# Kernel tuning notes

Hardware: AMD Instinct MI355X
Metric: run time of the kernel (lower is better)

The kernel has to match this reference:

```python
import jax, jax.numpy as jnp
import numpy as np
from jax.scipy.special import logsumexp

# K particles, J proposal candidates, N taxa, R merges done, T current subtrees,
# S sites, A alphabet, D embedding dim
K, J, N, R, T, S, A, D = 128, 4, 64, 32, 32, 256, 4, 64
PRIOR_BL = 0.1       # expected branch length under exponential prior
TEMPERATURE = 1.0


def _gather_nodes(arr, idx):
    # arr: (Z, t, ...); idx: (Z,) -> (Z, ...)  (per-row gather, gather_K)
    i = idx.reshape((-1,) + (1,) * (arr.ndim - 1))
    return jnp.take_along_axis(arr, i, axis=1)[:, 0]


def _replace_with_merged(arr, idx1, idx2, new_val):
    # remove nodes idx1, idx2 from each row (keeping order) and append merged node
    t = arr.shape[1]
    pos = jnp.arange(t)
    removed = (pos[None, :] == idx1[:, None]) | (pos[None, :] == idx2[:, None])
    order = jnp.argsort(removed.astype(jnp.int32), axis=1, stable=True)
    kept = order[:, : t - 2]
    ki = kept.reshape(kept.shape + (1,) * (arr.ndim - 2))
    kept_vals = jnp.take_along_axis(arr, ki, axis=1)
    return jnp.concatenate([kept_vals, new_val[:, None]], axis=1)


def _hash_tree(h1, h2):
    # order-invariant int32 hash combine (wraps on overflow, as intended)
    mn = jnp.minimum(h1, h2)
    mx = jnp.maximum(h1, h2)
    return (mn * 1000003 + mx) * 40503 + 2531011


def _q_matrix(emb_ZxD, W_q):
    # GTR-style rate matrix from merged-node embedding (site-independent decoder)
    logits = (emb_ZxD @ W_q).reshape(-1, A, A)
    off = jax.nn.softplus(logits) * (1.0 - jnp.eye(A, dtype=logits.dtype))
    return off - jnp.eye(A, dtype=logits.dtype) * off.sum(-1, keepdims=True)


def setup_inputs() -> dict:
    key = jax.random.key(0)
    ks = jax.random.split(key, 20)
    merge1_indexes_Kxr = jax.random.randint(ks[0], (K, R), 0, N).astype(jnp.int32)
    merge2_indexes_Kxr = jax.random.randint(ks[1], (K, R), 0, N).astype(jnp.int32)
    branch1_lengths_Kxr = jax.random.uniform(ks[2], (K, R)) * 0.2 + 1e-3
    branch2_lengths_Kxr = jax.random.uniform(ks[3], (K, R)) * 0.2 + 1e-3
    embeddings_KxrxD = jax.random.normal(ks[4], (K, R, D))
    # leaf counts per subtree, summing to N per particle
    lc_row = jnp.concatenate([jnp.full((T // 2,), 1, jnp.int32), jnp.full((T - T // 2,), 3, jnp.int32)])
    leaf_counts_Kxt = jnp.tile(lc_row[None], (K, 1))
    hashes_Kxt = jax.random.randint(ks[5], (K, T), 0, 2 ** 30).astype(jnp.int32)
    embeddings_KxtxD = jax.random.normal(ks[6], (K, T, D))
    log_felsensteins_KxtxSxA = -jax.random.uniform(ks[7], (K, T, S, A)) * 3.0
    log_pi_K = -jax.random.uniform(ks[8], (K,)) * 100.0
    indexes_K = jax.random.randint(ks[9], (K,), 0, K).astype(jnp.int32)
    # proposal outputs (stand-in for the learned proposal): idx1 != idx2
    idx1_KxJ = jax.random.randint(ks[10], (K, J), 0, T).astype(jnp.int32)
    off = jax.random.randint(ks[11], (K, J), 1, T).astype(jnp.int32)
    idx2_KxJ = (idx1_KxJ + off) % T
    branch1_KxJ = jax.random.uniform(ks[12], (K, J)) * 0.2 + 1e-3
    branch2_KxJ = jax.random.uniform(ks[13], (K, J)) * 0.2 + 1e-3
    embedding_KxJxD = jax.random.normal(ks[14], (K, J, D))
    log_v_plus_KxJ = jnp.full((K, J), np.log(T * (T - 1) / 2.0), jnp.float32)
    gumbel_KxJ = jax.random.gumbel(ks[15], (K, J))
    W_q = jax.random.normal(ks[16], (D, A * A)) * 0.05
    W_stat = jax.random.normal(ks[17], (D, A)) * 0.05
    vals = np.zeros(2 * N, dtype=np.float64)
    for i in range(2, 2 * N):
        vals[i] = vals[i - 2] + np.log(i)
    log_double_factorials_2N = jnp.asarray(vals, jnp.float32)
    return {
        'indexes_K': indexes_K,
        'merge1_indexes_Kxr': merge1_indexes_Kxr,
        'merge2_indexes_Kxr': merge2_indexes_Kxr,
        'branch1_lengths_Kxr': branch1_lengths_Kxr,
        'branch2_lengths_Kxr': branch2_lengths_Kxr,
        'embeddings_KxrxD': embeddings_KxrxD,
        'leaf_counts_Kxt': leaf_counts_Kxt,
        'hashes_Kxt': hashes_Kxt,
        'embeddings_KxtxD': embeddings_KxtxD,
        'log_felsensteins_KxtxSxA': log_felsensteins_KxtxSxA,
        'log_pi_K': log_pi_K,
        'idx1_KxJ': idx1_KxJ,
        'idx2_KxJ': idx2_KxJ,
        'branch1_KxJ': branch1_KxJ,
        'branch2_KxJ': branch2_KxJ,
        'embedding_KxJxD': embedding_KxJxD,
        'log_v_plus_KxJ': log_v_plus_KxJ,
        'gumbel_KxJ': gumbel_KxJ,
        'W_q': W_q,
        'W_stat': W_stat,
        'log_double_factorials_2N': log_double_factorials_2N,
    }


def reference(indexes_K, merge1_indexes_Kxr, merge2_indexes_Kxr,
              branch1_lengths_Kxr, branch2_lengths_Kxr, embeddings_KxrxD,
              leaf_counts_Kxt, hashes_Kxt, embeddings_KxtxD,
              log_felsensteins_KxtxSxA, log_pi_K,
              idx1_KxJ, idx2_KxJ, branch1_KxJ, branch2_KxJ,
              embedding_KxJxD, log_v_plus_KxJ, gumbel_KxJ,
              W_q, W_stat, log_double_factorials_2N):
    # ---- ancestor resampling gather (ms[...][indexes_K]) ----
    g = lambda a: a[indexes_K]
    merge1_Kxr = g(merge1_indexes_Kxr); merge2_Kxr = g(merge2_indexes_Kxr)
    b1_Kxr = g(branch1_lengths_Kxr); b2_Kxr = g(branch2_lengths_Kxr)
    emb_KxrxD = g(embeddings_KxrxD)
    lc_Kxt = g(leaf_counts_Kxt); h_Kxt = g(hashes_Kxt)
    emb_KxtxD = g(embeddings_KxtxD)
    lf_KxtxSxA = g(log_felsensteins_KxtxSxA)
    logpi_K = g(log_pi_K)
    # ---- flatten proposal to Z = K*J (hash_trick=False: Z = K*J, no dedup) ----
    Z = K * J
    rep = lambda a: jnp.repeat(a, J, axis=0)  # K_to_Z
    idx1_Z = idx1_KxJ.reshape(Z); idx2_Z = idx2_KxJ.reshape(Z)
    branch1_Z = branch1_KxJ.reshape(Z); branch2_Z = branch2_KxJ.reshape(Z)
    emb_ZxD = embedding_KxJxD.reshape(Z, D)
    log_v_plus_Z = log_v_plus_KxJ.reshape(Z)
    merge1_Z = rep(merge1_Kxr); merge2_Z = rep(merge2_Kxr)
    b1_Z = rep(b1_Kxr); b2_Z = rep(b2_Kxr)
    embr_Z = rep(emb_KxrxD)
    lc_Z = rep(lc_Kxt); h_Z = rep(h_Kxt)
    embt_Z = rep(emb_KxtxD)
    lf_Z = rep(lf_KxtxSxA)
    logpi_Z = rep(logpi_K)
    # ---- append candidate branches ----
    b1_all = jnp.concatenate([b1_Z, branch1_Z[:, None]], axis=1)  # Z x (R+1)
    b2_all = jnp.concatenate([b2_Z, branch2_Z[:, None]], axis=1)
    # ---- merge step ----
    new_lc = _gather_nodes(lc_Z, idx1_Z) + _gather_nodes(lc_Z, idx2_Z)
    new_h = _hash_tree(_gather_nodes(h_Z, idx1_Z), _gather_nodes(h_Z, idx2_Z))
    lc_new = _replace_with_merged(lc_Z, idx1_Z, idx2_Z, new_lc)      # Z x (T-1)
    h_new = _replace_with_merged(h_Z, idx1_Z, idx2_Z, new_h)
    embt_new = _replace_with_merged(embt_Z, idx1_Z, idx2_Z, emb_ZxD)
    # ---- Felsenstein pruning update ----
    Q = _q_matrix(emb_ZxD, W_q)                                      # Z x A x A
    expm = jax.scipy.linalg.expm
    P1 = jax.vmap(expm)(Q * branch1_Z[:, None, None])
    P2 = jax.vmap(expm)(Q * branch2_Z[:, None, None])
    logP1 = jnp.log(jnp.clip(P1, 1e-30))
    logP2 = jnp.log(jnp.clip(P2, 1e-30))
    lf1 = _gather_nodes(lf_Z, idx1_Z)  # Z x S x A
    lf2 = _gather_nodes(lf_Z, idx2_Z)
    new_lf = (logsumexp(logP1[:, None, :, :] + lf1[:, :, None, :], axis=-1)
              + logsumexp(logP2[:, None, :, :] + lf2[:, :, None, :], axis=-1))
    lf_new = _replace_with_merged(lf_Z, idx1_Z, idx2_Z, new_lf)      # Z x (T-1) x S x A
    # ---- stationary probs per node & log pi ----
    log_stat = jax.nn.log_softmax(embt_new @ W_stat, axis=-1)        # Z x (T-1) x A
    ll_nodes = logsumexp(lf_new + log_stat[:, :, None, :], axis=-1).sum(-1)  # Z x (T-1)
    log_lik_Z = ll_nodes.sum(-1)
    rate = 1.0 / PRIOR_BL
    log_branch_prior = ((jnp.log(rate) - rate * b1_all).sum(-1)
                        + (jnp.log(rate) - rate * b2_all).sum(-1))
    df_idx = jnp.clip(2 * lc_new - 3, 0, 2 * N - 1)
    log_topo = -log_double_factorials_2N[df_idx].sum(-1)
    log_pi_new_Z = log_lik_Z + log_branch_prior + log_topo
    log_v_minus_Z = jnp.log(jnp.sum(lc_new > 1, axis=-1).astype(jnp.float32))
    # ---- weights & sub-resampling ----
    log_w_Z = log_pi_new_Z - logpi_Z + log_v_minus_Z - log_v_plus_Z
    log_w_KxJ = log_w_Z.reshape(K, J)
    log_weight_K = logsumexp(log_w_KxJ, axis=1) - jnp.log(float(J))
    sub_idx_K = jnp.argmax(log_w_KxJ / TEMPERATURE + gumbel_KxJ, axis=1)  # Gumbel-max = Categorical sample
    sel = jnp.arange(K) * J + sub_idx_K
    gs = lambda a: a[sel]
    merge1_out = jnp.concatenate([gs(merge1_Z), gs(idx1_Z)[:, None]], axis=1)
    merge2_out = jnp.concatenate([gs(merge2_Z), gs(idx2_Z)[:, None]], axis=1)
    embr_out = jnp.concatenate([gs(embr_Z), gs(emb_ZxD)[:, None, :]], axis=1)
    return (merge1_out, merge2_out, gs(b1_all), gs(b2_all), embr_out,
            gs(lc_new), gs(h_new), gs(embt_new), gs(lf_new),
            gs(log_pi_new_Z), log_weight_K, gs(log_lik_Z))
```

## Files before the change

kernel.cpp:

```cpp
#include <hip/hip_runtime.h>
#include <math.h>

constexpr int K_ = 128, J_ = 4, R_ = 32, T_ = 32, S_ = 256, A_ = 4, D_ = 64;
constexpr int Z_ = K_ * J_;
constexpr int NDF_ = 128;
constexpr float RATE_ = 10.0f;

constexpr int NB_NODE = K_ * T_ / 4;
constexpr int NB_HYP  = Z_ / 4;

constexpr int OFF_M1   = 0;
constexpr int OFF_M2   = OFF_M1 + K_ * 33;
constexpr int OFF_B1   = OFF_M2 + K_ * 33;
constexpr int OFF_B2   = OFF_B1 + K_ * 33;
constexpr int OFF_EMBR = OFF_B2 + K_ * 33;
constexpr int OFF_LC   = OFF_EMBR + K_ * 33 * D_;
constexpr int OFF_H    = OFF_LC + K_ * 31;
constexpr int OFF_EMBT = OFF_H + K_ * 31;
constexpr int OFF_LF   = OFF_EMBT + K_ * 31 * D_;
constexpr int OFF_LPN  = OFF_LF + K_ * 31 * S_ * A_;
constexpr int OFF_LW   = OFF_LPN + K_;
constexpr int OFF_LL   = OFF_LW + K_;


__device__ inline float lse4f(float a, float b, float c, float d) {
    float m = fmaxf(fmaxf(a, b), fmaxf(c, d));
    return m + __logf(__expf(a - m) + __expf(b - m) + __expf(c - m) + __expf(d - m));
}

__global__ __launch_bounds__(256) void k_main(
    const int* __restrict__ indexes, const float* __restrict__ embt,
    const float* __restrict__ Wstat, const float* __restrict__ lf,
    const int* __restrict__ idx1_KJ, const int* __restrict__ idx2_KJ,
    const float* __restrict__ br1_KJ, const float* __restrict__ br2_KJ,
    const float* __restrict__ emb_KJD, const float* __restrict__ Wq,
    float* __restrict__ node_ll, float* __restrict__ new_node_ll,
    float* __restrict__ logP_ws) {
    int blk = blockIdx.x;
    int tid = threadIdx.x;
    int wave = tid >> 6, lane = tid & 63;

    if (blk < NB_NODE) {
        int kt = blk * 4 + wave;
        int k = kt >> 5, t = kt & 31;
        int src = indexes[k];
        float e = embt[(src * T_ + t) * D_ + lane];
        const float4 w4 = *(const float4*)&Wstat[lane * 4];
        float g0 = e * w4.x, g1 = e * w4.y, g2 = e * w4.z, g3 = e * w4.w;
#pragma unroll
        for (int m = 32; m; m >>= 1) {
            g0 += __shfl_xor(g0, m, 64);
            g1 += __shfl_xor(g1, m, 64);
            g2 += __shfl_xor(g2, m, 64);
            g3 += __shfl_xor(g3, m, 64);
        }
        float lse = lse4f(g0, g1, g2, g3);
        float ls0 = g0 - lse, ls1 = g1 - lse, ls2 = g2 - lse, ls3 = g3 - lse;
        const float4* fr = (const float4*)&lf[((size_t)(src * T_ + t) * S_ + lane * 4) * A_];
        double acc = 0.0;
#pragma unroll
        for (int s4 = 0; s4 < 4; ++s4) {
            float4 f = fr[s4];
            acc += (double)lse4f(f.x + ls0, f.y + ls1, f.z + ls2, f.w + ls3);
        }
#pragma unroll
        for (int m = 32; m; m >>= 1) acc += __shfl_xor(acc, m, 64);
        if (lane == 0) node_ll[kt] = (float)acc;
    } else {
        int z = (blk - NB_NODE) * 4 + wave;
        int k = z >> 2;
        int src = indexes[k];
        int i1 = idx1_KJ[z], i2 = idx2_KJ[z];

        __shared__ float s_val[4][20];
        __shared__ float s_logP[4][32];

        const float* emb = &emb_KJD[z * D_];
        if (lane < 16) {
            float lg = 0.f;
            for (int d = 0; d < D_; ++d) lg += emb[d] * Wq[d * 16 + lane];
            s_val[wave][lane] = lg;
        } else if (lane < 20) {
            int a = lane - 16;
            float lg = 0.f;
            for (int d = 0; d < D_; ++d) lg += emb[d] * Wstat[d * 4 + a];
            s_val[wave][lane] = lg;
        }
        __syncthreads();

        if (lane < 8) {
            int h = lane >> 2, r = lane & 3;
            int base = h * 4;
            double q[16];
#pragma unroll
            for (int i = 0; i < 4; ++i) {
                double rs = 0.0;
#pragma unroll
                for (int j = 0; j < 4; ++j) {
                    if (i != j) {
                        double x = (double)s_val[wave][i * 4 + j];
                        double sp = (x > 30.0) ? x : log1p(exp(x));
                        q[i * 4 + j] = sp;
                        rs += sp;
                    }
                }
                q[i * 4 + i] = -rs;
            }
            double br = (double)(h == 0 ? br1_KJ[z] : br2_KJ[z]);
            double c = br * (1.0 / 64.0);
#pragma unroll
            for (int e2 = 0; e2 < 16; ++e2) q[e2] *= c;
            double trow[4], arow[4];
#pragma unroll
            for (int j = 0; j < 4; ++j) { trow[j] = (j == r) ? 1.0 : 0.0; arow[j] = trow[j]; }
            const double inv_n[11] = {0.0, 1.0, 0.5, 1.0 / 3.0, 0.25, 0.2,
                                      1.0 / 6.0, 1.0 / 7.0, 0.125, 1.0 / 9.0, 0.1};
#pragma unroll
            for (int n = 1; n <= 10; ++n) {
                double nt[4];
#pragma unroll
                for (int j = 0; j < 4; ++j)
                    nt[j] = (trow[0] * q[0 * 4 + j] + trow[1] * q[1 * 4 + j] +
                             trow[2] * q[2 * 4 + j] + trow[3] * q[3 * 4 + j]) * inv_n[n];
#pragma unroll
                for (int j = 0; j < 4; ++j) { trow[j] = nt[j]; arow[j] += nt[j]; }
            }
#pragma unroll
            for (int sq = 0; sq < 6; ++sq) {
                double nrow[4];
#pragma unroll
                for (int j = 0; j < 4; ++j) {
                    double aj = arow[j];
                    nrow[j] = arow[0] * __shfl(aj, base + 0, 64)
                            + arow[1] * __shfl(aj, base + 1, 64)
                            + arow[2] * __shfl(aj, base + 2, 64)
                            + arow[3] * __shfl(aj, base + 3, 64);
                }
#pragma unroll
                for (int j = 0; j < 4; ++j) arow[j] = nrow[j];
            }
#pragma unroll
            for (int j = 0; j < 4; ++j) {
                float pf = (float)fmax(arow[j], 1e-30);
                float lv = __logf(pf);
                s_logP[wave][h * 16 + r * 4 + j] = lv;
                logP_ws[z * 32 + h * 16 + r * 4 + j] = lv;
            }
        }
        __syncthreads();

        float sl0 = s_val[wave][16], sl1 = s_val[wave][17];
        float sl2 = s_val[wave][18], sl3 = s_val[wave][19];
        float lseS = lse4f(sl0, sl1, sl2, sl3);
        float ls0 = sl0 - lseS, ls1 = sl1 - lseS, ls2 = sl2 - lseS, ls3 = sl3 - lseS;
        float p1[16], p2[16];
#pragma unroll
        for (int i = 0; i < 16; ++i) { p1[i] = s_logP[wave][i]; p2[i] = s_logP[wave][16 + i]; }
        const float4* f1p = (const float4*)&lf[((size_t)(src * T_ + i1) * S_ + lane * 4) * A_];
        const float4* f2p = (const float4*)&lf[((size_t)(src * T_ + i2) * S_ + lane * 4) * A_];
        double acc = 0.0;
#pragma unroll
        for (int s4 = 0; s4 < 4; ++s4) {
            float4 f = f1p[s4];
            float4 g = f2p[s4];
            float nlf[4];
#pragma unroll
            for (int a = 0; a < 4; ++a) {
                float t1 = lse4f(p1[a * 4 + 0] + f.x, p1[a * 4 + 1] + f.y,
                                 p1[a * 4 + 2] + f.z, p1[a * 4 + 3] + f.w);
                float t2 = lse4f(p2[a * 4 + 0] + g.x, p2[a * 4 + 1] + g.y,
                                 p2[a * 4 + 2] + g.z, p2[a * 4 + 3] + g.w);
                nlf[a] = t1 + t2;
            }
            acc += (double)lse4f(nlf[0] + ls0, nlf[1] + ls1, nlf[2] + ls2, nlf[3] + ls3);
        }
#pragma unroll
        for (int m = 32; m; m >>= 1) acc += __shfl_xor(acc, m, 64);
        if (lane == 0) new_node_ll[z] = (float)acc;
    }
}

__global__ __launch_bounds__(64) void k_finalize(
    const int* __restrict__ indexes, const int* __restrict__ lc_Kt,
    const float* __restrict__ b1_Kr, const float* __restrict__ b2_Kr,
    const float* __restrict__ logpi_K, const int* __restrict__ idx1_KJ,
    const int* __restrict__ idx2_KJ, const float* __restrict__ br1_KJ,
    const float* __restrict__ br2_KJ, const float* __restrict__ logvp_KJ,
    const float* __restrict__ gumbel_KJ, const float* __restrict__ ldf,
    const float* __restrict__ node_ll, const float* __restrict__ new_node_ll,
    float* __restrict__ out, int* __restrict__ sub_idx) {
    int k = blockIdx.x;
    int lane = threadIdx.x;
    int src = indexes[k];
    double nll = 0.0, topo = 0.0, sb1 = 0.0, sb2 = 0.0;
    int cnt = 0;
    if (lane < T_) {
        nll = (double)node_ll[k * T_ + lane];
        int lc = lc_Kt[src * T_ + lane];
        int di = 2 * lc - 3; di = max(0, min(NDF_ - 1, di));
        topo = (double)ldf[di];
        cnt = (lc > 1) ? 1 : 0;
        sb1 = (double)b1_Kr[src * R_ + lane];
        sb2 = (double)b2_Kr[src * R_ + lane];
    }
    for (int o = 32; o > 0; o >>= 1) {
        nll += __shfl_down(nll, o, 64);
        topo += __shfl_down(topo, o, 64);
        sb1 += __shfl_down(sb1, o, 64);
        sb2 += __shfl_down(sb2, o, 64);
        cnt += __shfl_down(cnt, o, 64);
    }
    if (lane == 0) {
        double total_ll = nll, base_topo = -topo;
        const double lr = log(10.0);
        double lw[4], lpn[4], llik[4];
        for (int j = 0; j < J_; ++j) {
            int z = k * J_ + j;
            int i1 = idx1_KJ[z], i2 = idx2_KJ[z];
            int lc1 = lc_Kt[src * T_ + i1], lc2 = lc_Kt[src * T_ + i2];
            int nlc = lc1 + lc2;
            double loglik = total_ll - (double)node_ll[k * T_ + i1]
                                     - (double)node_ll[k * T_ + i2]
                                     + (double)new_node_ll[z];
            double lbp = 66.0 * lr
                       - (double)RATE_ * (sb1 + (double)br1_KJ[z] + sb2 + (double)br2_KJ[z]);
            int d1 = max(0, min(NDF_ - 1, 2 * lc1 - 3));
            int d2 = max(0, min(NDF_ - 1, 2 * lc2 - 3));
            int dn = max(0, min(NDF_ - 1, 2 * nlc - 3));
            double lt = base_topo + (double)ldf[d1] + (double)ldf[d2] - (double)ldf[dn];
            int cntj = cnt - ((lc1 > 1) ? 1 : 0) - ((lc2 > 1) ? 1 : 0) + 1;
            double lvm = log((double)cntj);
            lpn[j] = loglik + lbp + lt;
            llik[j] = loglik;
            lw[j] = lpn[j] - (double)logpi_K[src] + lvm - (double)logvp_KJ[z];
        }
        double m = fmax(fmax(lw[0], lw[1]), fmax(lw[2], lw[3]));
        double ssum = exp(lw[0] - m) + exp(lw[1] - m) + exp(lw[2] - m) + exp(lw[3] - m);
        double logw = m + log(ssum) - log((double)J_);
        int best = 0;
        double bv = lw[0] + (double)gumbel_KJ[k * J_ + 0];
        for (int j = 1; j < J_; ++j) {
            double v = lw[j] + (double)gumbel_KJ[k * J_ + j];
            if (v > bv) { bv = v; best = j; }
        }
        out[OFF_LPN + k] = (float)lpn[best];
        out[OFF_LW + k] = (float)logw;
        out[OFF_LL + k] = (float)llik[best];
        sub_idx[k] = best;
    }
}

__global__ __launch_bounds__(256) void k_output(
    const int* __restrict__ indexes, const int* __restrict__ m1_Kr,
    const int* __restrict__ m2_Kr, const float* __restrict__ b1_Kr,
    const float* __restrict__ b2_Kr, const float* __restrict__ embr,
    const int* __restrict__ lc_Kt, const int* __restrict__ h_Kt,
    const float* __restrict__ embt, const float* __restrict__ lf,
    const int* __restrict__ idx1_KJ, const int* __restrict__ idx2_KJ,
    const float* __restrict__ br1_KJ, const float* __restrict__ br2_KJ,
    const float* __restrict__ emb_KJD, const float* __restrict__ logP_ws,
    const int* __restrict__ sub_idx, float* __restrict__ out) {
    int blk = blockIdx.x;
    int k = blk >> 5, part = blk & 31;
    int tid = threadIdx.x;
    int src = indexes[k];
    int sub = sub_idx[k];
    int z = k * J_ + sub;
    int i1 = idx1_KJ[z], i2 = idx2_KJ[z];
    int mn = min(i1, i2), mx = max(i1, i2);

    if (part < 30) {
        int st = part;
        if (st >= mn) ++st;
        if (st >= mx) ++st;
        const float4 v = *(const float4*)&lf[((size_t)(src * T_ + st) * S_ + tid) * A_];
        *(float4*)&out[OFF_LF + ((size_t)(k * 31 + part) * S_ + tid) * A_] = v;
    } else if (part == 30) {
        __shared__ float s_logP[32];
        if (tid < 32) s_logP[tid] = logP_ws[z * 32 + tid];
        __syncthreads();
        const float4 f1 = *(const float4*)&lf[((size_t)(src * T_ + i1) * S_ + tid) * A_];
        const float4 f2 = *(const float4*)&lf[((size_t)(src * T_ + i2) * S_ + tid) * A_];
        float4 o4;
        float nlf[4];
#pragma unroll
        for (int a = 0; a < 4; ++a) {
            float t1 = lse4f(s_logP[a * 4 + 0] + f1.x, s_logP[a * 4 + 1] + f1.y,
                             s_logP[a * 4 + 2] + f1.z, s_logP[a * 4 + 3] + f1.w);
            float t2 = lse4f(s_logP[16 + a * 4 + 0] + f2.x, s_logP[16 + a * 4 + 1] + f2.y,
                             s_logP[16 + a * 4 + 2] + f2.z, s_logP[16 + a * 4 + 3] + f2.w);
            nlf[a] = t1 + t2;
        }
        o4.x = nlf[0]; o4.y = nlf[1]; o4.z = nlf[2]; o4.w = nlf[3];
        *(float4*)&out[OFF_LF + ((size_t)(k * 31 + 30) * S_ + tid) * A_] = o4;
    } else {
        for (int i = tid; i < 33; i += 256) {
            float v1, v2, fb1, fb2;
            if (i < 32) {
                v1 = (float)m1_Kr[src * R_ + i];
                v2 = (float)m2_Kr[src * R_ + i];
                fb1 = b1_Kr[src * R_ + i];
                fb2 = b2_Kr[src * R_ + i];
            } else {
                v1 = (float)i1; v2 = (float)i2;
                fb1 = br1_KJ[z]; fb2 = br2_KJ[z];
            }
            out[OFF_M1 + k * 33 + i] = v1;
            out[OFF_M2 + k * 33 + i] = v2;
            out[OFF_B1 + k * 33 + i] = fb1;
            out[OFF_B2 + k * 33 + i] = fb2;
        }
        for (int i = tid; i < 33 * D_; i += 256) {
            int r = i >> 6, d = i & 63;
            float v = (r < 32) ? embr[(src * R_ + r) * D_ + d] : emb_KJD[z * D_ + d];
            out[OFF_EMBR + k * 33 * D_ + i] = v;
        }
        for (int i = tid; i < 31; i += 256) {
            int lcv, hv;
            if (i < 30) {
                int st = i;
                if (st >= mn) ++st;
                if (st >= mx) ++st;
                lcv = lc_Kt[src * T_ + st];
                hv = h_Kt[src * T_ + st];
            } else {
                lcv = lc_Kt[src * T_ + i1] + lc_Kt[src * T_ + i2];
                int h1 = h_Kt[src * T_ + i1], h2 = h_Kt[src * T_ + i2];
                int hmn = min(h1, h2), hmx = max(h1, h2);
                unsigned int u = ((unsigned int)hmn * 1000003u + (unsigned int)hmx) * 40503u
                                 + 2531011u;
                hv = (int)u;
            }
            out[OFF_LC + k * 31 + i] = (float)lcv;
            out[OFF_H + k * 31 + i] = (float)hv;
        }
        for (int i = tid; i < 31 * D_; i += 256) {
            int t = i >> 6, d = i & 63;
            float v;
            if (t < 30) {
                int st = t;
                if (st >= mn) ++st;
                if (st >= mx) ++st;
                v = embt[(src * T_ + st) * D_ + d];
            } else {
                v = emb_KJD[z * D_ + d];
            }
            out[OFF_EMBT + k * 31 * D_ + i] = v;
        }
    }
}

extern "C" void kernel_launch(void* const* d_in, const int* in_sizes, int n_in,
                              void* d_out, int out_size, void* d_ws, size_t ws_size,
                              hipStream_t stream) {
    const int* indexes   = (const int*)d_in[0];
    const int* m1_Kr     = (const int*)d_in[1];
    const int* m2_Kr     = (const int*)d_in[2];
    const float* b1_Kr   = (const float*)d_in[3];
    const float* b2_Kr   = (const float*)d_in[4];
    const float* embr    = (const float*)d_in[5];
    const int* lc_Kt     = (const int*)d_in[6];
    const int* h_Kt      = (const int*)d_in[7];
    const float* embt    = (const float*)d_in[8];
    const float* lf      = (const float*)d_in[9];
    const float* logpi_K = (const float*)d_in[10];
    const int* idx1_KJ   = (const int*)d_in[11];
    const int* idx2_KJ   = (const int*)d_in[12];
    const float* br1_KJ  = (const float*)d_in[13];
    const float* br2_KJ  = (const float*)d_in[14];
    const float* emb_KJD = (const float*)d_in[15];
    const float* logvp_KJ = (const float*)d_in[16];
    const float* gumbel_KJ = (const float*)d_in[17];
    const float* Wq      = (const float*)d_in[18];
    const float* Wstat   = (const float*)d_in[19];
    const float* ldf     = (const float*)d_in[20];

    float* out = (float*)d_out;
    float* ws_f = (float*)d_ws;
    float* new_node_ll = ws_f;
    float* node_ll = ws_f + Z_;
    int* sub_idx = (int*)(ws_f + Z_ + K_ * T_);
    float* logP_ws = ws_f + Z_ + K_ * T_ + K_;

    k_main<<<NB_NODE + NB_HYP, 256, 0, stream>>>(
        indexes, embt, Wstat, lf, idx1_KJ, idx2_KJ, br1_KJ, br2_KJ, emb_KJD, Wq,
        node_ll, new_node_ll, logP_ws);
    k_finalize<<<K_, 64, 0, stream>>>(indexes, lc_Kt, b1_Kr, b2_Kr, logpi_K, idx1_KJ,
                                      idx2_KJ, br1_KJ, br2_KJ, logvp_KJ, gumbel_KJ,
                                      ldf, node_ll, new_node_ll, out, sub_idx);
    k_output<<<K_ * 32, 256, 0, stream>>>(indexes, m1_Kr, m2_Kr, b1_Kr, b2_Kr, embr,
                                          lc_Kt, h_Kt, embt, lf, idx1_KJ, idx2_KJ,
                                          br1_KJ, br2_KJ, emb_KJD, logP_ws, sub_idx, out);
}
```

Measured before the change: 155.8 us.

## Fuse three kernels into one per-particle kernel with in-block resampling

Merges the node-likelihood, finalize and output kernels into a single kernel with one 256-thread block per particle, keeping node likelihoods, hypothesis likelihoods, logP matrices and the selected index in shared memory instead of workspace. It also switches the Q-matrix exponential from double to float, computes the decoder logits with a wave-wide shuffle reduction instead of serial loops, and coalesces the lf reads. This removes two launch gaps and the global round trips, but leaves only 128 blocks, each doing serial work including a 30-row copy loop, so the GPU may be underused and memory bandwidth poorly covered. Float precision in the matrix exponential may change numerical accuracy.

After: 146.6 us. 5.9% less time.

```diff
diff --git a/kernel.cpp b/kernel.cpp
--- a/kernel.cpp
+++ b/kernel.cpp
@@ -2,12 +2,8 @@
 #include <math.h>
 
 constexpr int K_ = 128, J_ = 4, R_ = 32, T_ = 32, S_ = 256, A_ = 4, D_ = 64;
-constexpr int Z_ = K_ * J_;
 constexpr int NDF_ = 128;
 constexpr float RATE_ = 10.0f;
-
-constexpr int NB_NODE = K_ * T_ / 4;
-constexpr int NB_HYP  = Z_ / 4;
 
 constexpr int OFF_M1   = 0;
 constexpr int OFF_M2   = OFF_M1 + K_ * 33;
@@ -22,28 +18,36 @@
 constexpr int OFF_LW   = OFF_LPN + K_;
 constexpr int OFF_LL   = OFF_LW + K_;
 
-
 __device__ inline float lse4f(float a, float b, float c, float d) {
     float m = fmaxf(fmaxf(a, b), fmaxf(c, d));
     return m + __logf(__expf(a - m) + __expf(b - m) + __expf(c - m) + __expf(d - m));
 }
 
-__global__ __launch_bounds__(256) void k_main(
-    const int* __restrict__ indexes, const float* __restrict__ embt,
-    const float* __restrict__ Wstat, const float* __restrict__ lf,
-    const int* __restrict__ idx1_KJ, const int* __restrict__ idx2_KJ,
-    const float* __restrict__ br1_KJ, const float* __restrict__ br2_KJ,
-    const float* __restrict__ emb_KJD, const float* __restrict__ Wq,
-    float* __restrict__ node_ll, float* __restrict__ new_node_ll,
-    float* __restrict__ logP_ws) {
-    int blk = blockIdx.x;
+__global__ __launch_bounds__(256) void k_all(
+    const int* __restrict__ indexes, const int* __restrict__ m1_Kr,
+    const int* __restrict__ m2_Kr, const float* __restrict__ b1_Kr,
+    const float* __restrict__ b2_Kr, const float* __restrict__ embr,
+    const int* __restrict__ lc_Kt, const int* __restrict__ h_Kt,
+    const float* __restrict__ embt, const float* __restrict__ lf,
+    const float* __restrict__ logpi_K, const int* __restrict__ idx1_KJ,
+    const int* __restrict__ idx2_KJ, const float* __restrict__ br1_KJ,
+    const float* __restrict__ br2_KJ, const float* __restrict__ emb_KJD,
+    const float* __restrict__ logvp_KJ, const float* __restrict__ gumbel_KJ,
+    const float* __restrict__ Wq, const float* __restrict__ Wstat,
+    const float* __restrict__ ldf, float* __restrict__ out) {
+    int k = blockIdx.x;
     int tid = threadIdx.x;
-    int wave = tid >> 6, lane = tid & 63;
-
-    if (blk < NB_NODE) {
-        int kt = blk * 4 + wave;
-        int k = kt >> 5, t = kt & 31;
-        int src = indexes[k];
+    int w = tid >> 6, lane = tid & 63;
+    int src = indexes[k];
+
+    __shared__ float s_node_ll[T_];
+    __shared__ float s_new_ll[J_];
+    __shared__ float s_logP[J_][32];
+    __shared__ int s_sub;
+
+#pragma unroll
+    for (int i = 0; i < 8; ++i) {
+        int t = i * 4 + w;
         float e = embt[(src * T_ + t) * D_ + lane];
         const float4 w4 = *(const float4*)&Wstat[lane * 4];
         float g0 = e * w4.x, g1 = e * w4.y, g2 = e * w4.z, g3 = e * w4.w;
@@ -56,68 +60,71 @@
         }
         float lse = lse4f(g0, g1, g2, g3);
         float ls0 = g0 - lse, ls1 = g1 - lse, ls2 = g2 - lse, ls3 = g3 - lse;
-        const float4* fr = (const float4*)&lf[((size_t)(src * T_ + t) * S_ + lane * 4) * A_];
+        const float4* fr = (const float4*)&lf[(size_t)(src * T_ + t) * S_ * A_];
         double acc = 0.0;
 #pragma unroll
         for (int s4 = 0; s4 < 4; ++s4) {
-            float4 f = fr[s4];
+            float4 f = fr[s4 * 64 + lane];
             acc += (double)lse4f(f.x + ls0, f.y + ls1, f.z + ls2, f.w + ls3);
         }
 #pragma unroll
         for (int m = 32; m; m >>= 1) acc += __shfl_xor(acc, m, 64);
-        if (lane == 0) node_ll[kt] = (float)acc;
-    } else {
-        int z = (blk - NB_NODE) * 4 + wave;
-        int k = z >> 2;
-        int src = indexes[k];
+        if (lane == 0) s_node_ll[t] = (float)acc;
+    }
+
+    {
+        int z = k * J_ + w;
         int i1 = idx1_KJ[z], i2 = idx2_KJ[z];
 
-        __shared__ float s_val[4][20];
-        __shared__ float s_logP[4][32];
-
-        const float* emb = &emb_KJD[z * D_];
-        if (lane < 16) {
-            float lg = 0.f;
-            for (int d = 0; d < D_; ++d) lg += emb[d] * Wq[d * 16 + lane];
-            s_val[wave][lane] = lg;
-        } else if (lane < 20) {
-            int a = lane - 16;
-            float lg = 0.f;
-            for (int d = 0; d < D_; ++d) lg += emb[d] * Wstat[d * 4 + a];
-            s_val[wave][lane] = lg;
-        }
-        __syncthreads();
-
+        float emb_d = emb_KJD[z * D_ + lane];
+        float lg[20];
+        const float4* wqr = (const float4*)&Wq[lane * 16];
+        float4 q0 = wqr[0], q1 = wqr[1], q2 = wqr[2], q3 = wqr[3];
+        lg[0] = emb_d * q0.x;  lg[1] = emb_d * q0.y;  lg[2] = emb_d * q0.z;  lg[3] = emb_d * q0.w;
+        lg[4] = emb_d * q1.x;  lg[5] = emb_d * q1.y;  lg[6] = emb_d * q1.z;  lg[7] = emb_d * q1.w;
+        lg[8] = emb_d * q2.x;  lg[9] = emb_d * q2.y;  lg[10] = emb_d * q2.z; lg[11] = emb_d * q2.w;
+        lg[12] = emb_d * q3.x; lg[13] = emb_d * q3.y; lg[14] = emb_d * q3.z; lg[15] = emb_d * q3.w;
+        const float4 ws4 = *(const float4*)&Wstat[lane * 4];
+        lg[16] = emb_d * ws4.x; lg[17] = emb_d * ws4.y; lg[18] = emb_d * ws4.z; lg[19] = emb_d * ws4.w;
+#pragma unroll
+        for (int m = 32; m; m >>= 1) {
+#pragma unroll
+            for (int p = 0; p < 20; ++p) lg[p] += __shfl_xor(lg[p], m, 64);
+        }
+
+        float lseS = lse4f(lg[16], lg[17], lg[18], lg[19]);
+        float ls0 = lg[16] - lseS, ls1 = lg[17] - lseS, ls2 = lg[18] - lseS, ls3 = lg[19] - lseS;
+
+        float lv[4] = {0.f, 0.f, 0.f, 0.f};
         if (lane < 8) {
-            int h = lane >> 2, r = lane & 3;
-            int base = h * 4;
-            double q[16];
+            int h = lane >> 2, r = lane & 3, base = h * 4;
+            float q[16];
 #pragma unroll
             for (int i = 0; i < 4; ++i) {
-                double rs = 0.0;
+                float rs = 0.f;
 #pragma unroll
                 for (int j = 0; j < 4; ++j) {
                     if (i != j) {
-                        double x = (double)s_val[wave][i * 4 + j];
-                        double sp = (x > 30.0) ? x : log1p(exp(x));
+                        float x = lg[i * 4 + j];
+                        float sp = (x > 15.f) ? x : log1pf(__expf(x));
                         q[i * 4 + j] = sp;
                         rs += sp;
                     }
                 }
                 q[i * 4 + i] = -rs;
             }
-            double br = (double)(h == 0 ? br1_KJ[z] : br2_KJ[z]);
-            double c = br * (1.0 / 64.0);
+            float br = (h == 0) ? br1_KJ[z] : br2_KJ[z];
+            float c = br * (1.f / 64.f);
 #pragma unroll
             for (int e2 = 0; e2 < 16; ++e2) q[e2] *= c;
-            double trow[4], arow[4];
-#pragma unroll
-            for (int j = 0; j < 4; ++j) { trow[j] = (j == r) ? 1.0 : 0.0; arow[j] = trow[j]; }
-            const double inv_n[11] = {0.0, 1.0, 0.5, 1.0 / 3.0, 0.25, 0.2,
-                                      1.0 / 6.0, 1.0 / 7.0, 0.125, 1.0 / 9.0, 0.1};
+            float trow[4], arow[4];
+#pragma unroll
+            for (int j = 0; j < 4; ++j) { trow[j] = (j == r) ? 1.f : 0.f; arow[j] = trow[j]; }
+            const float inv_n[11] = {0.f, 1.f, 0.5f, 1.f / 3.f, 0.25f, 0.2f,
+                                     1.f / 6.f, 1.f / 7.f, 0.125f, 1.f / 9.f, 0.1f};
 #pragma unroll
             for (int n = 1; n <= 10; ++n) {
-                double nt[4];
+                float nt[4];
 #pragma unroll
                 for (int j = 0; j < 4; ++j)
                     nt[j] = (trow[0] * q[0 * 4 + j] + trow[1] * q[1 * 4 + j] +
@@ -127,10 +134,10 @@
             }
 #pragma unroll
             for (int sq = 0; sq < 6; ++sq) {
-                double nrow[4];
+                float nrow[4];
 #pragma unroll
                 for (int j = 0; j < 4; ++j) {
-                    double aj = arow[j];
+                    float aj = arow[j];
                     nrow[j] = arow[0] * __shfl(aj, base + 0, 64)
                             + arow[1] * __shfl(aj, base + 1, 64)
                             + arow[2] * __shfl(aj, base + 2, 64)
@@ -141,28 +148,26 @@
             }
 #pragma unroll
             for (int j = 0; j < 4; ++j) {
-                float pf = (float)fmax(arow[j], 1e-30);
-                float lv = __logf(pf);
-                s_logP[wave][h * 16 + r * 4 + j] = lv;
-                logP_ws[z * 32 + h * 16 + r * 4 + j] = lv;
-            }
-        }
-        __syncthreads();
-
-        float sl0 = s_val[wave][16], sl1 = s_val[wave][17];
-        float sl2 = s_val[wave][18], sl3 = s_val[wave][19];
-        float lseS = lse4f(sl0, sl1, sl2, sl3);
-        float ls0 = sl0 - lseS, ls1 = sl1 - lseS, ls2 = sl2 - lseS, ls3 = sl3 - lseS;
+                lv[j] = __logf(fmaxf(arow[j], 1e-30f));
+                s_logP[w][h * 16 + r * 4 + j] = lv[j];
+            }
+        }
         float p1[16], p2[16];
 #pragma unroll
-        for (int i = 0; i < 16; ++i) { p1[i] = s_logP[wave][i]; p2[i] = s_logP[wave][16 + i]; }
-        const float4* f1p = (const float4*)&lf[((size_t)(src * T_ + i1) * S_ + lane * 4) * A_];
-        const float4* f2p = (const float4*)&lf[((size_t)(src * T_ + i2) * S_ + lane * 4) * A_];
+        for (int r = 0; r < 4; ++r) {
+#pragma unroll
+            for (int j = 0; j < 4; ++j) {
+                p1[r * 4 + j] = __shfl(lv[j], r, 64);
+                p2[r * 4 + j] = __shfl(lv[j], 4 + r, 64);
+            }
+        }
+        const float4* f1p = (const float4*)&lf[(size_t)(src * T_ + i1) * S_ * A_];
+        const float4* f2p = (const float4*)&lf[(size_t)(src * T_ + i2) * S_ * A_];
         double acc = 0.0;
 #pragma unroll
         for (int s4 = 0; s4 < 4; ++s4) {
-            float4 f = f1p[s4];
-            float4 g = f2p[s4];
+            float4 f = f1p[s4 * 64 + lane];
+            float4 g = f2p[s4 * 64 + lane];
             float nlf[4];
 #pragma unroll
             for (int a = 0; a < 4; ++a) {
@@ -176,177 +181,150 @@
         }
 #pragma unroll
         for (int m = 32; m; m >>= 1) acc += __shfl_xor(acc, m, 64);
-        if (lane == 0) new_node_ll[z] = (float)acc;
-    }
-}
-
-__global__ __launch_bounds__(64) void k_finalize(
-    const int* __restrict__ indexes, const int* __restrict__ lc_Kt,
-    const float* __restrict__ b1_Kr, const float* __restrict__ b2_Kr,
-    const float* __restrict__ logpi_K, const int* __restrict__ idx1_KJ,
-    const int* __restrict__ idx2_KJ, const float* __restrict__ br1_KJ,
-    const float* __restrict__ br2_KJ, const float* __restrict__ logvp_KJ,
-    const float* __restrict__ gumbel_KJ, const float* __restrict__ ldf,
-    const float* __restrict__ node_ll, const float* __restrict__ new_node_ll,
-    float* __restrict__ out, int* __restrict__ sub_idx) {
-    int k = blockIdx.x;
-    int lane = threadIdx.x;
-    int src = indexes[k];
-    double nll = 0.0, topo = 0.0, sb1 = 0.0, sb2 = 0.0;
-    int cnt = 0;
-    if (lane < T_) {
-        nll = (double)node_ll[k * T_ + lane];
-        int lc = lc_Kt[src * T_ + lane];
-        int di = 2 * lc - 3; di = max(0, min(NDF_ - 1, di));
-        topo = (double)ldf[di];
-        cnt = (lc > 1) ? 1 : 0;
-        sb1 = (double)b1_Kr[src * R_ + lane];
-        sb2 = (double)b2_Kr[src * R_ + lane];
-    }
-    for (int o = 32; o > 0; o >>= 1) {
-        nll += __shfl_down(nll, o, 64);
-        topo += __shfl_down(topo, o, 64);
-        sb1 += __shfl_down(sb1, o, 64);
-        sb2 += __shfl_down(sb2, o, 64);
-        cnt += __shfl_down(cnt, o, 64);
-    }
-    if (lane == 0) {
-        double total_ll = nll, base_topo = -topo;
-        const double lr = log(10.0);
-        double lw[4], lpn[4], llik[4];
-        for (int j = 0; j < J_; ++j) {
-            int z = k * J_ + j;
-            int i1 = idx1_KJ[z], i2 = idx2_KJ[z];
-            int lc1 = lc_Kt[src * T_ + i1], lc2 = lc_Kt[src * T_ + i2];
-            int nlc = lc1 + lc2;
-            double loglik = total_ll - (double)node_ll[k * T_ + i1]
-                                     - (double)node_ll[k * T_ + i2]
-                                     + (double)new_node_ll[z];
-            double lbp = 66.0 * lr
-                       - (double)RATE_ * (sb1 + (double)br1_KJ[z] + sb2 + (double)br2_KJ[z]);
-            int d1 = max(0, min(NDF_ - 1, 2 * lc1 - 3));
-            int d2 = max(0, min(NDF_ - 1, 2 * lc2 - 3));
-            int dn = max(0, min(NDF_ - 1, 2 * nlc - 3));
-            double lt = base_topo + (double)ldf[d1] + (double)ldf[d2] - (double)ldf[dn];
-            int cntj = cnt - ((lc1 > 1) ? 1 : 0) - ((lc2 > 1) ? 1 : 0) + 1;
-            double lvm = log((double)cntj);
-            lpn[j] = loglik + lbp + lt;
-            llik[j] = loglik;
-            lw[j] = lpn[j] - (double)logpi_K[src] + lvm - (double)logvp_KJ[z];
-        }
-        double m = fmax(fmax(lw[0], lw[1]), fmax(lw[2], lw[3]));
-        double ssum = exp(lw[0] - m) + exp(lw[1] - m) + exp(lw[2] - m) + exp(lw[3] - m);
-        double logw = m + log(ssum) - log((double)J_);
-        int best = 0;
-        double bv = lw[0] + (double)gumbel_KJ[k * J_ + 0];
-        for (int j = 1; j < J_; ++j) {
-            double v = lw[j] + (double)gumbel_KJ[k * J_ + j];
-            if (v > bv) { bv = v; best = j; }
-        }
-        out[OFF_LPN + k] = (float)lpn[best];
-        out[OFF_LW + k] = (float)logw;
-        out[OFF_LL + k] = (float)llik[best];
-        sub_idx[k] = best;
-    }
-}
-
-__global__ __launch_bounds__(256) void k_output(
-    const int* __restrict__ indexes, const int* __restrict__ m1_Kr,
-    const int* __restrict__ m2_Kr, const float* __restrict__ b1_Kr,
-    const float* __restrict__ b2_Kr, const float* __restrict__ embr,
-    const int* __restrict__ lc_Kt, const int* __restrict__ h_Kt,
-    const float* __restrict__ embt, const float* __restrict__ lf,
-    const int* __restrict__ idx1_KJ, const int* __restrict__ idx2_KJ,
-    const float* __restrict__ br1_KJ, const float* __restrict__ br2_KJ,
-    const float* __restrict__ emb_KJD, const float* __restrict__ logP_ws,
-    const int* __restrict__ sub_idx, float* __restrict__ out) {
-    int blk = blockIdx.x;
-    int k = blk >> 5, part = blk & 31;
-    int tid = threadIdx.x;
-    int src = indexes[k];
-    int sub = sub_idx[k];
-    int z = k * J_ + sub;
-    int i1 = idx1_KJ[z], i2 = idx2_KJ[z];
-    int mn = min(i1, i2), mx = max(i1, i2);
-
-    if (part < 30) {
-        int st = part;
+        if (lane == 0) s_new_ll[w] = (float)acc;
+    }
+    __syncthreads();
+
+    if (w == 0) {
+        double nll = 0.0, topo = 0.0, sb1 = 0.0, sb2 = 0.0;
+        int cnt = 0;
+        if (lane < T_) {
+            nll = (double)s_node_ll[lane];
+            int lc = lc_Kt[src * T_ + lane];
+            int di = 2 * lc - 3; di = max(0, min(NDF_ - 1, di));
+            topo = (double)ldf[di];
+            cnt = (lc > 1) ? 1 : 0;
+            sb1 = (double)b1_Kr[src * R_ + lane];
+            sb2 = (double)b2_Kr[src * R_ + lane];
+        }
+        for (int o = 32; o > 0; o >>= 1) {
+            nll += __shfl_down(nll, o, 64);
+            topo += __shfl_down(topo, o, 64);
+            sb1 += __shfl_down(sb1, o, 64);
+            sb2 += __shfl_down(sb2, o, 64);
+            cnt += __shfl_down(cnt, o, 64);
+        }
+        if (lane == 0) {
+            double total_ll = nll, base_topo = -topo;
+            const double lr = log(10.0);
+            double lw[4], lpn[4], llik[4];
+            for (int j = 0; j < J_; ++j) {
+                int z = k * J_ + j;
+                int i1 = idx1_KJ[z], i2 = idx2_KJ[z];
+                int lc1 = lc_Kt[src * T_ + i1], lc2 = lc_Kt[src * T_ + i2];
+                int nlc = lc1 + lc2;
+                double loglik = total_ll - (double)s_node_ll[i1] - (double)s_node_ll[i2]
+                              + (double)s_new_ll[j];
+                double lbp = 66.0 * lr
+                           - (double)RATE_ * (sb1 + (double)br1_KJ[z] + sb2 + (double)br2_KJ[z]);
+                int d1 = max(0, min(NDF_ - 1, 2 * lc1 - 3));
+                int d2 = max(0, min(NDF_ - 1, 2 * lc2 - 3));
+                int dn = max(0, min(NDF_ - 1, 2 * nlc - 3));
+                double lt = base_topo + (double)ldf[d1] + (double)ldf[d2] - (double)ldf[dn];
+                int cntj = cnt - ((lc1 > 1) ? 1 : 0) - ((lc2 > 1) ? 1 : 0) + 1;
+                double lvm = log((double)cntj);
+                lpn[j] = loglik + lbp + lt;
+                llik[j] = loglik;
+                lw[j] = lpn[j] - (double)logpi_K[src] + lvm - (double)logvp_KJ[z];
+            }
+            double m = fmax(fmax(lw[0], lw[1]), fmax(lw[2], lw[3]));
+            double ssum = exp(lw[0] - m) + exp(lw[1] - m) + exp(lw[2] - m) + exp(lw[3] - m);
+            double logw = m + log(ssum) - log((double)J_);
+            int best = 0;
+            double bv = lw[0] + (double)gumbel_KJ[k * J_ + 0];
+            for (int j = 1; j < J_; ++j) {
+                double v = lw[j] + (double)gumbel_KJ[k * J_ + j];
+                if (v > bv) { bv = v; best = j; }
+            }
+            out[OFF_LPN + k] = (float)lpn[best];
+            out[OFF_LW + k] = (float)logw;
+            out[OFF_LL + k] = (float)llik[best];
+            s_sub = best;
+        }
+    }
+    __syncthreads();
+
+    int sub = s_sub;
+    int zs = k * J_ + sub;
+    int si1 = idx1_KJ[zs], si2 = idx2_KJ[zs];
+    int mn = min(si1, si2), mx = max(si1, si2);
+
+    {
+        float P1[16], P2[16];
+#pragma unroll
+        for (int i = 0; i < 16; ++i) { P1[i] = s_logP[sub][i]; P2[i] = s_logP[sub][16 + i]; }
+        const float4 f1 = *(const float4*)&lf[((size_t)(src * T_ + si1) * S_ + tid) * A_];
+        const float4 f2 = *(const float4*)&lf[((size_t)(src * T_ + si2) * S_ + tid) * A_];
+        float4 o4;
+#pragma unroll
+        for (int a = 0; a < 4; ++a) {
+            float t1 = lse4f(P1[a * 4 + 0] + f1.x, P1[a * 4 + 1] + f1.y,
+                             P1[a * 4 + 2] + f1.z, P1[a * 4 + 3] + f1.w);
+            float t2 = lse4f(P2[a * 4 + 0] + f2.x, P2[a * 4 + 1] + f2.y,
+                             P2[a * 4 + 2] + f2.z, P2[a * 4 + 3] + f2.w);
+            ((float*)&o4)[a] = t1 + t2;
+        }
+        *(float4*)&out[OFF_LF + ((size_t)(k * 31 + 30) * S_ + tid) * A_] = o4;
+    }
+    for (int row = 0; row < 30; ++row) {
+        int st = row;
         if (st >= mn) ++st;
         if (st >= mx) ++st;
         const float4 v = *(const float4*)&lf[((size_t)(src * T_ + st) * S_ + tid) * A_];
-        *(float4*)&out[OFF_LF + ((size_t)(k * 31 + part) * S_ + tid) * A_] = v;
-    } else if (part == 30) {
-        __shared__ float s_logP[32];
-        if (tid < 32) s_logP[tid] = logP_ws[z * 32 + tid];
-        __syncthreads();
-        const float4 f1 = *(const float4*)&lf[((size_t)(src * T_ + i1) * S_ + tid) * A_];
-        const float4 f2 = *(const float4*)&lf[((size_t)(src * T_ + i2) * S_ + tid) * A_];
-        float4 o4;
-        float nlf[4];
-#pragma unroll
-        for (int a = 0; a < 4; ++a) {
-            float t1 = lse4f(s_logP[a * 4 + 0] + f1.x, s_logP[a * 4 + 1] + f1.y,
-                             s_logP[a * 4 + 2] + f1.z, s_logP[a * 4 + 3] + f1.w);
-            float t2 = lse4f(s_logP[16 + a * 4 + 0] + f2.x, s_logP[16 + a * 4 + 1] + f2.y,
-                             s_logP[16 + a * 4 + 2] + f2.z, s_logP[16 + a * 4 + 3] + f2.w);
-            nlf[a] = t1 + t2;
-        }
-        o4.x = nlf[0]; o4.y = nlf[1]; o4.z = nlf[2]; o4.w = nlf[3];
-        *(float4*)&out[OFF_LF + ((size_t)(k * 31 + 30) * S_ + tid) * A_] = o4;
-    } else {
-        for (int i = tid; i < 33; i += 256) {
-            float v1, v2, fb1, fb2;
-            if (i < 32) {
-                v1 = (float)m1_Kr[src * R_ + i];
-                v2 = (float)m2_Kr[src * R_ + i];
-                fb1 = b1_Kr[src * R_ + i];
-                fb2 = b2_Kr[src * R_ + i];
-            } else {
-                v1 = (float)i1; v2 = (float)i2;
-                fb1 = br1_KJ[z]; fb2 = br2_KJ[z];
-            }
-            out[OFF_M1 + k * 33 + i] = v1;
-            out[OFF_M2 + k * 33 + i] = v2;
-            out[OFF_B1 + k * 33 + i] = fb1;
-            out[OFF_B2 + k * 33 + i] = fb2;
-        }
-        for (int i = tid; i < 33 * D_; i += 256) {
-            int r = i >> 6, d = i & 63;
-            float v = (r < 32) ? embr[(src * R_ + r) * D_ + d] : emb_KJD[z * D_ + d];
-            out[OFF_EMBR + k * 33 * D_ + i] = v;
-        }
-        for (int i = tid; i < 31; i += 256) {
-            int lcv, hv;
-            if (i < 30) {
-                int st = i;
-                if (st >= mn) ++st;
-                if (st >= mx) ++st;
-                lcv = lc_Kt[src * T_ + st];
-                hv = h_Kt[src * T_ + st];
-            } else {
-                lcv = lc_Kt[src * T_ + i1] + lc_Kt[src * T_ + i2];
-                int h1 = h_Kt[src * T_ + i1], h2 = h_Kt[src * T_ + i2];
-                int hmn = min(h1, h2), hmx = max(h1, h2);
-                unsigned int u = ((unsigned int)hmn * 1000003u + (unsigned int)hmx) * 40503u
-                                 + 2531011u;
-                hv = (int)u;
-            }
-            out[OFF_LC + k * 31 + i] = (float)lcv;
-            out[OFF_H + k * 31 + i] = (float)hv;
-        }
-        for (int i = tid; i < 31 * D_; i += 256) {
-            int t = i >> 6, d = i & 63;
-            float v;
-            if (t < 30) {
-                int st = t;
-                if (st >= mn) ++st;
-                if (st >= mx) ++st;
-                v = embt[(src * T_ + st) * D_ + d];
-            } else {
-                v = emb_KJD[z * D_ + d];
-            }
-            out[OFF_EMBT + k * 31 * D_ + i] = v;
-        }
+        *(float4*)&out[OFF_LF + ((size_t)(k * 31 + row) * S_ + tid) * A_] = v;
+    }
+    for (int i = tid; i < 33; i += 256) {
+        float v1, v2, fb1, fb2;
+        if (i < 32) {
+            v1 = (float)m1_Kr[src * R_ + i];
+            v2 = (float)m2_Kr[src * R_ + i];
+            fb1 = b1_Kr[src * R_ + i];
+            fb2 = b2_Kr[src * R_ + i];
+        } else {
+            v1 = (float)si1; v2 = (float)si2;
+            fb1 = br1_KJ[zs]; fb2 = br2_KJ[zs];
+        }
+        out[OFF_M1 + k * 33 + i] = v1;
+        out[OFF_M2 + k * 33 + i] = v2;
+        out[OFF_B1 + k * 33 + i] = fb1;
+        out[OFF_B2 + k * 33 + i] = fb2;
+    }
+    for (int i = tid; i < 33 * D_; i += 256) {
+        int r = i >> 6, d = i & 63;
+        float v = (r < 32) ? embr[(src * R_ + r) * D_ + d] : emb_KJD[zs * D_ + d];
+        out[OFF_EMBR + k * 33 * D_ + i] = v;
+    }
+    for (int i = tid; i < 31; i += 256) {
+        int lcv, hv;
+        if (i < 30) {
+            int st = i;
+            if (st >= mn) ++st;
+            if (st >= mx) ++st;
+            lcv = lc_Kt[src * T_ + st];
+            hv = h_Kt[src * T_ + st];
+        } else {
+            lcv = lc_Kt[src * T_ + si1] + lc_Kt[src * T_ + si2];
+            int h1 = h_Kt[src * T_ + si1], h2 = h_Kt[src * T_ + si2];
+            int hmn = min(h1, h2), hmx = max(h1, h2);
+            unsigned int u = ((unsigned int)hmn * 1000003u + (unsigned int)hmx) * 40503u
+                             + 2531011u;
+            hv = (int)u;
+        }
+        out[OFF_LC + k * 31 + i] = (float)lcv;
+        out[OFF_H + k * 31 + i] = (float)hv;
+    }
+    for (int i = tid; i < 31 * D_; i += 256) {
+        int t = i >> 6, d = i & 63;
+        float v;
+        if (t < 30) {
+            int st = t;
+            if (st >= mn) ++st;
+            if (st >= mx) ++st;
+            v = embt[(src * T_ + st) * D_ + d];
+        } else {
+            v = emb_KJD[zs * D_ + d];
+        }
+        out[OFF_EMBT + k * 31 * D_ + i] = v;
     }
 }
 
@@ -374,21 +352,10 @@
     const float* Wq      = (const float*)d_in[18];
     const float* Wstat   = (const float*)d_in[19];
     const float* ldf     = (const float*)d_in[20];
-
     float* out = (float*)d_out;
-    float* ws_f = (float*)d_ws;
-    float* new_node_ll = ws_f;
-    float* node_ll = ws_f + Z_;
-    int* sub_idx = (int*)(ws_f + Z_ + K_ * T_);
-    float* logP_ws = ws_f + Z_ + K_ * T_ + K_;
-
-    k_main<<<NB_NODE + NB_HYP, 256, 0, stream>>>(
-        indexes, embt, Wstat, lf, idx1_KJ, idx2_KJ, br1_KJ, br2_KJ, emb_KJD, Wq,
-        node_ll, new_node_ll, logP_ws);
-    k_finalize<<<K_, 64, 0, stream>>>(indexes, lc_Kt, b1_Kr, b2_Kr, logpi_K, idx1_KJ,
-                                      idx2_KJ, br1_KJ, br2_KJ, logvp_KJ, gumbel_KJ,
-                                      ldf, node_ll, new_node_ll, out, sub_idx);
-    k_output<<<K_ * 32, 256, 0, stream>>>(indexes, m1_Kr, m2_Kr, b1_Kr, b2_Kr, embr,
-                                          lc_Kt, h_Kt, embt, lf, idx1_KJ, idx2_KJ,
-                                          br1_KJ, br2_KJ, emb_KJD, logP_ws, sub_idx, out);
+
+    k_all<<<K_, 256, 0, stream>>>(indexes, m1_Kr, m2_Kr, b1_Kr, b2_Kr, embr,
+                                  lc_Kt, h_Kt, embt, lf, logpi_K, idx1_KJ, idx2_KJ,
+                                  br1_KJ, br2_KJ, emb_KJD, logvp_KJ, gumbel_KJ,
+                                  Wq, Wstat, ldf, out);
 }
```

## Use float matrix exponential, wave-parallel logits, coalesced site loads, no LDS syncs

Applied to the files above, without the earlier changes.

The hypothesis branch now computes the 20 logits by having each lane take one embedding dimension and reducing across the wave with shuffles, where before 20 lanes each ran a serial 64-step loop. The transition-matrix exponential (Taylor series plus squaring) is done in fp32 instead of fp64. Shared memory and both __syncthreads are gone, and log-probabilities are broadcast with shuffles instead. Partial-likelihood loads are changed to a lane-contiguous float4 stride for coalescing, which changes which sites each lane covers but not the total sum. The fp32 switch and the lower softplus cutoff reduce precision of logP.

New measurement: 147.6 us. 1.06x faster.

```diff
diff --git a/kernel.cpp b/kernel.cpp
--- a/kernel.cpp
+++ b/kernel.cpp
@@ -22,13 +22,12 @@
 constexpr int OFF_LW   = OFF_LPN + K_;
 constexpr int OFF_LL   = OFF_LW + K_;
 
-
 __device__ inline float lse4f(float a, float b, float c, float d) {
     float m = fmaxf(fmaxf(a, b), fmaxf(c, d));
     return m + __logf(__expf(a - m) + __expf(b - m) + __expf(c - m) + __expf(d - m));
 }
 
-__global__ __launch_bounds__(256) void k_main(
+__global__ __launch_bounds__(256) void k_compute(
     const int* __restrict__ indexes, const float* __restrict__ embt,
     const float* __restrict__ Wstat, const float* __restrict__ lf,
     const int* __restrict__ idx1_KJ, const int* __restrict__ idx2_KJ,
@@ -38,10 +37,10 @@
     float* __restrict__ logP_ws) {
     int blk = blockIdx.x;
     int tid = threadIdx.x;
-    int wave = tid >> 6, lane = tid & 63;
+    int w = tid >> 6, lane = tid & 63;
 
     if (blk < NB_NODE) {
-        int kt = blk * 4 + wave;
+        int kt = blk * 4 + w;
         int k = kt >> 5, t = kt & 31;
         int src = indexes[k];
         float e = embt[(src * T_ + t) * D_ + lane];
@@ -56,68 +55,71 @@
         }
         float lse = lse4f(g0, g1, g2, g3);
         float ls0 = g0 - lse, ls1 = g1 - lse, ls2 = g2 - lse, ls3 = g3 - lse;
-        const float4* fr = (const float4*)&lf[((size_t)(src * T_ + t) * S_ + lane * 4) * A_];
+        const float4* fr = (const float4*)&lf[(size_t)(src * T_ + t) * S_ * A_];
         double acc = 0.0;
 #pragma unroll
         for (int s4 = 0; s4 < 4; ++s4) {
-            float4 f = fr[s4];
+            float4 f = fr[s4 * 64 + lane];
             acc += (double)lse4f(f.x + ls0, f.y + ls1, f.z + ls2, f.w + ls3);
         }
 #pragma unroll
         for (int m = 32; m; m >>= 1) acc += __shfl_xor(acc, m, 64);
         if (lane == 0) node_ll[kt] = (float)acc;
     } else {
-        int z = (blk - NB_NODE) * 4 + wave;
+        int z = (blk - NB_NODE) * 4 + w;
         int k = z >> 2;
         int src = indexes[k];
         int i1 = idx1_KJ[z], i2 = idx2_KJ[z];
 
-        __shared__ float s_val[4][20];
-        __shared__ float s_logP[4][32];
-
-        const float* emb = &emb_KJD[z * D_];
-        if (lane < 16) {
-            float lg = 0.f;
-            for (int d = 0; d < D_; ++d) lg += emb[d] * Wq[d * 16 + lane];
-            s_val[wave][lane] = lg;
-        } else if (lane < 20) {
-            int a = lane - 16;
-            float lg = 0.f;
-            for (int d = 0; d < D_; ++d) lg += emb[d] * Wstat[d * 4 + a];
-            s_val[wave][lane] = lg;
-        }
-        __syncthreads();
-
+        float emb_d = emb_KJD[z * D_ + lane];
+        float lg[20];
+        const float4* wqr = (const float4*)&Wq[lane * 16];
+        float4 q0 = wqr[0], q1 = wqr[1], q2 = wqr[2], q3 = wqr[3];
+        lg[0] = emb_d * q0.x;  lg[1] = emb_d * q0.y;  lg[2] = emb_d * q0.z;  lg[3] = emb_d * q0.w;
+        lg[4] = emb_d * q1.x;  lg[5] = emb_d * q1.y;  lg[6] = emb_d * q1.z;  lg[7] = emb_d * q1.w;
+        lg[8] = emb_d * q2.x;  lg[9] = emb_d * q2.y;  lg[10] = emb_d * q2.z; lg[11] = emb_d * q2.w;
+        lg[12] = emb_d * q3.x; lg[13] = emb_d * q3.y; lg[14] = emb_d * q3.z; lg[15] = emb_d * q3.w;
+        const float4 ws4 = *(const float4*)&Wstat[lane * 4];
+        lg[16] = emb_d * ws4.x; lg[17] = emb_d * ws4.y; lg[18] = emb_d * ws4.z; lg[19] = emb_d * ws4.w;
+#pragma unroll
+        for (int m = 32; m; m >>= 1) {
+#pragma unroll
+            for (int p = 0; p < 20; ++p) lg[p] += __shfl_xor(lg[p], m, 64);
+        }
+
+        float lseS = lse4f(lg[16], lg[17], lg[18], lg[19]);
+        float ls0 = lg[16] - lseS, ls1 = lg[17] - lseS, ls2 = lg[18] - lseS, ls3 = lg[19] - lseS;
+
+        float lv[4] = {0.f, 0.f, 0.f, 0.f};
         if (lane < 8) {
-            int h = lane >> 2, r = lane & 3;
-            int base = h * 4;
-            double q[16];
+            int h = lane >> 2, r = lane & 3, base = h * 4;
+            float q[16];
 #pragma unroll
             for (int i = 0; i < 4; ++i) {
-                double rs = 0.0;
+                float rs = 0.f;
 #pragma unroll
                 for (int j = 0; j < 4; ++j) {
                     if (i != j) {
-                        double x = (double)s_val[wave][i * 4 + j];
-                        double sp = (x > 30.0) ? x : log1p(exp(x));
+                        float x = lg[i * 4 + j];
+                        float sp = (x > 15.f) ? x : log1pf(__expf(x));
                         q[i * 4 + j] = sp;
                         rs += sp;
                     }
                 }
                 q[i * 4 + i] = -rs;
             }
-            double br = (double)(h == 0 ? br1_KJ[z] : br2_KJ[z]);
-            double c = br * (1.0 / 64.0);
+            float br = (h == 0) ? br1_KJ[z] : br2_KJ[z];
+            float c = br * (1.f / 64.f);
 #pragma unroll
             for (int e2 = 0; e2 < 16; ++e2) q[e2] *= c;
-            double trow[4], arow[4];
-#pragma unroll
-            for (int j = 0; j < 4; ++j) { trow[j] = (j == r) ? 1.0 : 0.0; arow[j] = trow[j]; }
-            const double inv_n[11] = {0.0, 1.0, 0.5, 1.0 / 3.0, 0.25, 0.2,
-                                      1.0 / 6.0, 1.0 / 7.0, 0.125, 1.0 / 9.0, 0.1};
+            float trow[4], arow[4];
+#pragma unroll
+            for (int j = 0; j < 4; ++j) { trow[j] = (j == r) ? 1.f : 0.f; arow[j] = trow[j]; }
+            const float inv_n[11] = {0.f, 1.f, 0.5f, 1.f / 3.f, 0.25f, 0.2f,
+                                     1.f / 6.f, 1.f / 7.f, 0.125f, 1.f / 9.f, 0.1f};
 #pragma unroll
             for (int n = 1; n <= 10; ++n) {
-                double nt[4];
+                float nt[4];
 #pragma unroll
                 for (int j = 0; j < 4; ++j)
                     nt[j] = (trow[0] * q[0 * 4 + j] + trow[1] * q[1 * 4 + j] +
@@ -127,10 +129,10 @@
             }
 #pragma unroll
             for (int sq = 0; sq < 6; ++sq) {
-                double nrow[4];
+                float nrow[4];
 #pragma unroll
                 for (int j = 0; j < 4; ++j) {
-                    double aj = arow[j];
+                    float aj = arow[j];
                     nrow[j] = arow[0] * __shfl(aj, base + 0, 64)
                             + arow[1] * __shfl(aj, base + 1, 64)
                             + arow[2] * __shfl(aj, base + 2, 64)
@@ -141,28 +143,26 @@
             }
 #pragma unroll
             for (int j = 0; j < 4; ++j) {
-                float pf = (float)fmax(arow[j], 1e-30);
-                float lv = __logf(pf);
-                s_logP[wave][h * 16 + r * 4 + j] = lv;
-                logP_ws[z * 32 + h * 16 + r * 4 + j] = lv;
-            }
-        }
-        __syncthreads();
-
-        float sl0 = s_val[wave][16], sl1 = s_val[wave][17];
-        float sl2 = s_val[wave][18], sl3 = s_val[wave][19];
-        float lseS = lse4f(sl0, sl1, sl2, sl3);
-        float ls0 = sl0 - lseS, ls1 = sl1 - lseS, ls2 = sl2 - lseS, ls3 = sl3 - lseS;
+                lv[j] = __logf(fmaxf(arow[j], 1e-30f));
+                logP_ws[z * 32 + h * 16 + r * 4 + j] = lv[j];
+            }
+        }
         float p1[16], p2[16];
 #pragma unroll
-        for (int i = 0; i < 16; ++i) { p1[i] = s_logP[wave][i]; p2[i] = s_logP[wave][16 + i]; }
-        const float4* f1p = (const float4*)&lf[((size_t)(src * T_ + i1) * S_ + lane * 4) * A_];
-        const float4* f2p = (const float4*)&lf[((size_t)(src * T_ + i2) * S_ + lane * 4) * A_];
+        for (int r = 0; r < 4; ++r) {
+#pragma unroll
+            for (int j = 0; j < 4; ++j) {
+                p1[r * 4 + j] = __shfl(lv[j], r, 64);
+                p2[r * 4 + j] = __shfl(lv[j], 4 + r, 64);
+            }
+        }
+        const float4* f1p = (const float4*)&lf[(size_t)(src * T_ + i1) * S_ * A_];
+        const float4* f2p = (const float4*)&lf[(size_t)(src * T_ + i2) * S_ * A_];
         double acc = 0.0;
 #pragma unroll
         for (int s4 = 0; s4 < 4; ++s4) {
-            float4 f = f1p[s4];
-            float4 g = f2p[s4];
+            float4 f = f1p[s4 * 64 + lane];
+            float4 g = f2p[s4 * 64 + lane];
             float nlf[4];
 #pragma unroll
             for (int a = 0; a < 4; ++a) {
@@ -382,7 +382,7 @@
     int* sub_idx = (int*)(ws_f + Z_ + K_ * T_);
     float* logP_ws = ws_f + Z_ + K_ * T_ + K_;
 
-    k_main<<<NB_NODE + NB_HYP, 256, 0, stream>>>(
+    k_compute<<<NB_NODE + NB_HYP, 256, 0, stream>>>(
         indexes, embt, Wstat, lf, idx1_KJ, idx2_KJ, br1_KJ, br2_KJ, emb_KJD, Wq,
         node_ll, new_node_ll, logP_ws);
     k_finalize<<<K_, 64, 0, stream>>>(indexes, lc_Kt, b1_Kr, b2_Kr, logpi_K, idx1_KJ,
```
